# Kernel optimization log

Measured on AMD Instinct MI355X. Metric: run time of the kernel, lower is better.

Reference implementation:

```python
import jax, jax.numpy as jnp
import numpy as np

SEQ_LEN = 1632   # L, divisible by K=12, Locc=4, mmse_block=12
UP = 8           # number of (user, port) entries (flattened dict)
B = 32           # batch_size
A = 64           # num_rx_ant
K = 12           # ktc=4 -> K=12
LOCC = 4         # ktc=4 -> Locc=4
BLK = 12         # mmse_block_size
SEARCH = 10      # delay_search_range = (-10, 10)
RHO = 0.9        # exponential channel-correlation model for default C matrix


def setup_inputs() -> dict:
    key = jax.random.key(0)
    k1, k2, k3 = jax.random.split(key, 3)
    return {
        "ls_real": jax.random.normal(k1, (UP, B, A, SEQ_LEN), jnp.float32),
        "ls_imag": jax.random.normal(k2, (UP, B, A, SEQ_LEN), jnp.float32),
        "cyclic_shifts": jax.random.randint(k3, (UP,), 0, K, dtype=jnp.int32),
    }


def _estimate_entry(ls, n_u_p):
    """Full per-(user,port) pipeline. ls: [B, A, L] complex64, n_u_p: scalar int."""
    L = ls.shape[-1]
    bsz, nant = ls.shape[0], ls.shape[1]
    ideal_peak = ((K - n_u_p) % K) * (L // K)           # scalar int

    # --- IFFT to time domain + per-sample power summed over antennas ---
    h_time = jnp.fft.ifft(ls, axis=-1)                   # [B, A, L]
    pwr = jnp.sum(jnp.abs(h_time) ** 2, axis=1)          # [B, L]

    # --- timing-offset search in a window around the ideal peak ---
    offsets = jnp.arange(-SEARCH, SEARCH + 1)            # [21]
    idxs = (ideal_peak + offsets) % L                    # [21]
    window = pwr[:, idxs]                                # [B, 21]
    toff = offsets[jnp.argmax(window, axis=1)]           # [B] int
    m = toff + ideal_peak                                # [B] int

    # --- phasor correction exp(j 2 pi m n / L) (modular for precision) ---
    nvec = jnp.arange(L)
    ang = (2.0 * jnp.pi / L) * ((m[:, None] * nvec[None, :]) % L).astype(jnp.float32)
    phas_m = jnp.exp(1j * ang)                           # [B, L] complex64
    h_shift = ls * phas_m[:, None, :]                    # [B, A, L]

    # --- OCC demux: average groups of Locc ---
    red = L // LOCC
    h_avg = h_shift.reshape(bsz, nant, red, LOCC).mean(axis=-1)  # [B, A, L/4]

    # --- linear interpolation back to length L (np.interp semantics) ---
    # original sample positions: (LOCC-1)/2 + i*LOCC  (uniform grid)
    t = jnp.arange(L, dtype=jnp.float32)
    p = jnp.clip((t - (LOCC - 1) / 2.0) / LOCC, 0.0, red - 1.0)  # clamped -> edge hold
    i0 = jnp.clip(jnp.floor(p).astype(jnp.int32), 0, red - 2)
    frac = (p - i0.astype(jnp.float32))                  # [L] real
    h_interp = (jnp.take(h_avg, i0, axis=-1) * (1.0 - frac)
                + jnp.take(h_avg, i0 + 1, axis=-1) * frac)       # [B, A, L]

    # torch code computes this under no_grad -> block gradients
    h_wr = jax.lax.stop_gradient(h_interp)

    # --- noise power estimated from frequency-domain LS estimate ---
    d = ls[..., 1:] - ls[..., :-1]
    noise_pw = jnp.mean(jnp.abs(d) ** 2, axis=(1, 2)) / 2.0      # [B]

    # --- block MMSE filter: W = C (C + sigma^2 I)^-1, C = rho^|i-j| ---
    ii = jnp.arange(BLK)
    C = (RHO ** jnp.abs(ii[:, None] - ii[None, :])).astype(jnp.float32)  # [12,12]
    eye = jnp.eye(BLK, dtype=jnp.float32)
    inv = jax.vmap(lambda s: jnp.linalg.inv(C + s * eye))(noise_pw)       # [B,12,12]
    W = jnp.einsum('ij,bjk->bik', C, inv).astype(jnp.complex64)           # [B,12,12]

    hb = h_wr.reshape(bsz, nant, L // BLK, BLK)
    out = jnp.einsum('bij,banj->bani', W, hb).reshape(bsz, nant, L)
    return out


def reference(ls_real, ls_imag, cyclic_shifts):
    ls = ls_real + 1j * ls_imag                          # [UP, B, A, L] complex64
    out = jax.vmap(_estimate_entry)(ls, cyclic_shifts)   # [UP, B, A, L] complex64
    return jnp.stack([out.real, out.imag], axis=-1)      # [UP, B, A, L, 2] float32
```

## Files before the change

kernel.cpp:

```cpp
#include <hip/hip_runtime.h>
#include <math.h>

#define L 1632
#define NUP 8
#define NB 32
#define NA 64
#define KK 12
#define NW 21
#define RED 408

__global__ __launch_bounds__(256) void k1_window(
    const float* __restrict__ lsr, const float* __restrict__ lsi,
    const int* __restrict__ cshift,
    float* __restrict__ winp, float* __restrict__ noisep)
{
    const int bid   = blockIdx.x;
    const int ub    = bid >> 4;
    const int chunk = bid & 15;
    const int u     = ub >> 5;
    const int tid   = threadIdx.x;
    const int wave  = tid >> 6;
    const int lane  = tid & 63;
    const int a     = chunk * 4 + wave;
    const int row   = (ub * NA + a) * L;

    const int shift = cshift[u];
    const int ip    = ((KK - shift) % KK) * (L / KK);
    int t0 = ip - 10;
    t0 = ((t0 % L) + L) % L;

    const float cph = (float)(2.0 * M_PI / (double)L);

    float accr[NW], acci[NW];
#pragma unroll
    for (int o = 0; o < NW; o++) { accr[o] = 0.0f; acci[o] = 0.0f; }
    float na = 0.0f;
    float carry_r = 0.0f, carry_i = 0.0f;

#define ELEM(XR, XI, N) { \
    const int idx0 = ((N) * t0) % L; \
    float s0, c0, s1, c1; \
    __sincosf(cph * (float)idx0, &s0, &c0); \
    __sincosf(cph * (float)(N),  &s1, &c1); \
    float yr = (XR) * c0 - (XI) * s0; \
    float yi = (XR) * s0 + (XI) * c0; \
    _Pragma("unroll") \
    for (int o = 0; o < NW; o++) { \
        accr[o] += yr; acci[o] += yi; \
        const float t_ = yr * c1 - yi * s1; \
        yi = yr * s1 + yi * c1; yr = t_; } }

    for (int k = 0; k < 7; k++) {
        const int nb  = 256 * k + 4 * lane;
        const bool act = (nb < L);
        float4 xr = make_float4(0.f, 0.f, 0.f, 0.f);
        float4 xi = make_float4(0.f, 0.f, 0.f, 0.f);
        if (act) {
            xr = *reinterpret_cast<const float4*>(lsr + row + nb);
            xi = *reinterpret_cast<const float4*>(lsi + row + nb);
        }
        const float c63r = __shfl(carry_r, 63);
        const float c63i = __shfl(carry_i, 63);
        const float upr  = __shfl_up(xr.w, 1);
        const float upi  = __shfl_up(xi.w, 1);
        const float pr   = (lane == 0) ? c63r : upr;
        const float pi   = (lane == 0) ? c63i : upi;
        if (act) {
            if (!(k == 0 && lane == 0)) {
                const float dr = xr.x - pr, di = xi.x - pi; na += dr * dr + di * di;
            }
            { const float dr = xr.y - xr.x, di = xi.y - xi.x; na += dr * dr + di * di; }
            { const float dr = xr.z - xr.y, di = xi.z - xi.y; na += dr * dr + di * di; }
            { const float dr = xr.w - xr.z, di = xi.w - xi.z; na += dr * dr + di * di; }
        }
        carry_r = xr.w; carry_i = xi.w;
        ELEM(xr.x, xi.x, nb + 0)
        ELEM(xr.y, xi.y, nb + 1)
        ELEM(xr.z, xi.z, nb + 2)
        ELEM(xr.w, xi.w, nb + 3)
    }
#undef ELEM

#pragma unroll
    for (int m = 1; m < 64; m <<= 1) {
#pragma unroll
        for (int o = 0; o < NW; o++) {
            accr[o] += __shfl_xor(accr[o], m);
            acci[o] += __shfl_xor(acci[o], m);
        }
        na += __shfl_xor(na, m);
    }

    if (lane == 0) {
#pragma unroll
        for (int o = 0; o < NW; o++)
            atomicAdd(&winp[ub * NW + o], accr[o] * accr[o] + acci[o] * acci[o]);
        atomicAdd(&noisep[ub], na);
    }
}

__global__ __launch_bounds__(192) void k2_wmat(
    const float* __restrict__ winp, const float* __restrict__ noisep,
    const int* __restrict__ cshift,
    float* __restrict__ Wout, int* __restrict__ mmOut)
{
    const int ub  = blockIdx.x;
    const int u   = ub >> 5;
    const int tid = threadIdx.x;
    __shared__ float win[NW];
    __shared__ float Cs[12][12];
    __shared__ float aug[12][25];
    __shared__ float snoise;

    if (tid < NW) win[tid] = winp[ub * NW + tid];
    if (tid == NW) snoise = noisep[ub] / (float)NA / (float)(L - 1) / 2.0f;
    if (tid >= 32 && tid < 32 + 144) {
        const int t = tid - 32;
        const int i = t / 12, j = t % 12;
        const int d = (i > j) ? (i - j) : (j - i);
        double v = 1.0;
        for (int k = 0; k < d; k++) v *= 0.9;
        Cs[i][j] = (float)v;
    }
    __syncthreads();

    if (tid < 144) {
        const int i = tid / 12, j = tid % 12;
        aug[i][j]      = Cs[i][j] + ((i == j) ? snoise : 0.0f);
        aug[i][12 + j] = (i == j) ? 1.0f : 0.0f;
    }
    __syncthreads();

    for (int k = 0; k < 12; k++) {
        float pv = 1.0f, rowkj = 0.0f;
        float fcol[12];
        if (tid < 24) {
            pv    = aug[k][k];
            rowkj = aug[k][tid];
#pragma unroll
            for (int i = 0; i < 12; i++) fcol[i] = aug[i][k];
        }
        __syncthreads();
        if (tid < 24) {
            const float nrm = rowkj / pv;
            aug[k][tid] = nrm;
#pragma unroll
            for (int i = 0; i < 12; i++)
                if (i != k) aug[i][tid] -= fcol[i] * nrm;
        }
        __syncthreads();
    }

    if (tid == 0) {
        float best = win[0];
        int bo = 0;
        for (int o = 1; o < NW; o++)
            if (win[o] > best) { best = win[o]; bo = o; }
        const int shift = cshift[u];
        const int ip = ((KK - shift) % KK) * (L / KK);
        const int m = ip + (bo - 10);
        mmOut[ub] = ((m % L) + L) % L;
    }

    if (tid < 144) {
        const int i = tid / 12, j = tid % 12;
        float w = 0.0f;
#pragma unroll
        for (int k = 0; k < 12; k++) w += Cs[i][k] * aug[k][12 + j];
        Wout[ub * 144 + tid] = w;
    }
}

__global__ __launch_bounds__(256) void k3_main(
    const float* __restrict__ lsr, const float* __restrict__ lsi,
    const float* __restrict__ Wall, const int* __restrict__ mmArr,
    float* __restrict__ out)
{
    const int bid = blockIdx.x;
    const int ub  = bid >> 6;
    const int row = bid * L;
    const int tid = threadIdx.x;
    __shared__ float2 havg[RED];
    __shared__ float2 hint[L];
    __shared__ float  Wl[144];
    if (tid < 144) Wl[tid] = Wall[ub * 144 + tid];
    const int mm = mmArr[ub];
    const float cph = (float)(2.0 * M_PI / (double)L);

    for (int r = tid; r < RED; r += 256) {
        const int base = 4 * r;
        const float4 xr = *reinterpret_cast<const float4*>(lsr + row + base);
        const float4 xi = *reinterpret_cast<const float4*>(lsi + row + base);
        int idx = (mm * base) % L;
        float ar = 0.0f, ai = 0.0f, sn, cs;
        __sincosf(cph * (float)idx, &sn, &cs);
        ar += xr.x * cs - xi.x * sn; ai += xr.x * sn + xi.x * cs;
        idx += mm; if (idx >= L) idx -= L;
        __sincosf(cph * (float)idx, &sn, &cs);
        ar += xr.y * cs - xi.y * sn; ai += xr.y * sn + xi.y * cs;
        idx += mm; if (idx >= L) idx -= L;
        __sincosf(cph * (float)idx, &sn, &cs);
        ar += xr.z * cs - xi.z * sn; ai += xr.z * sn + xi.z * cs;
        idx += mm; if (idx >= L) idx -= L;
        __sincosf(cph * (float)idx, &sn, &cs);
        ar += xr.w * cs - xi.w * sn; ai += xr.w * sn + xi.w * cs;
        havg[r] = make_float2(ar * 0.25f, ai * 0.25f);
    }
    __syncthreads();

    for (int t = tid; t < L; t += 256) {
        float p = ((float)t - 1.5f) * 0.25f;
        p = fminf(fmaxf(p, 0.0f), 407.0f);
        int i0 = (int)p;
        if (i0 > 406) i0 = 406;
        const float fr = p - (float)i0;
        const float2 h0 = havg[i0], h1 = havg[i0 + 1];
        hint[t] = make_float2(h0.x * (1.0f - fr) + h1.x * fr,
                              h0.y * (1.0f - fr) + h1.y * fr);
    }
    __syncthreads();

    float2* o2 = reinterpret_cast<float2*>(out);
    for (int e = tid; e < L; e += 256) {
        const int j = e / 12;
        const int i = e - j * 12;
        const float* wr = &Wl[i * 12];
        float ax = 0.0f, ay = 0.0f;
#pragma unroll
        for (int k = 0; k < 12; k++) {
            const float  w = wr[k];
            const float2 h = hint[j * 12 + k];
            ax += w * h.x; ay += w * h.y;
        }
        o2[row + e] = make_float2(ax, ay);
    }
}

extern "C" void kernel_launch(void* const* d_in, const int* in_sizes, int n_in,
                              void* d_out, int out_size, void* d_ws, size_t ws_size,
                              hipStream_t stream) {
    const float* lsr    = (const float*)d_in[0];
    const float* lsi    = (const float*)d_in[1];
    const int*   cshift = (const int*)d_in[2];
    float* out = (float*)d_out;

    char* ws = (char*)d_ws;
    float* Wout   = (float*)(ws);
    float* winp   = (float*)(ws + 147456);
    float* noisep = (float*)(ws + 147456 + 21504);
    int*   mmArr  = (int*)  (ws + 147456 + 21504 + 1024);

    hipMemsetAsync(winp, 0, 21504 + 1024, stream);

    hipLaunchKernelGGL(k1_window, dim3(NUP * NB * 16), dim3(256), 0, stream,
                       lsr, lsi, cshift, winp, noisep);
    hipLaunchKernelGGL(k2_wmat, dim3(NUP * NB), dim3(192), 0, stream,
                       winp, noisep, cshift, Wout, mmArr);
    hipLaunchKernelGGL(k3_main, dim3(NUP * NB * NA), dim3(256), 0, stream,
                       lsr, lsi, Wout, mmArr, out);
}
```

Baseline: 504.8 us.

## Compute windowed DFT via radix-4 split with shared-memory twiddle table

The k1 window kernel now splits each row into four quarter segments, combines them with a radix-4 butterfly, and evaluates the 21 DFT bins against a precomputed cos/sin table kept in shared memory. This replaces the per-element sincos calls and the 21-step rotation recurrence of the old version. Each block now handles one (user,batch) pair across all 64 antennas, with 8 waves each doing 8 antennas, so the per-bin results are reduced in shared memory and written directly. That removes the global atomics and the memset. The cost is a large shared-memory table (about 68KB) and only 256 blocks of 512 threads, which may leave the GPU underoccupied.

After: 605.6 us. +20.0%, slower.

```diff
diff --git a/kernel.cpp b/kernel.cpp
--- a/kernel.cpp
+++ b/kernel.cpp
@@ -8,21 +8,23 @@
 #define KK 12
 #define NW 21
 #define RED 408
-
-__global__ __launch_bounds__(256) void k1_window(
+#define WS 408
+#define WIM (NW*WS)
+
+__global__ __launch_bounds__(512, 2) void k1_window(
     const float* __restrict__ lsr, const float* __restrict__ lsi,
     const int* __restrict__ cshift,
     float* __restrict__ winp, float* __restrict__ noisep)
 {
-    const int bid   = blockIdx.x;
-    const int ub    = bid >> 4;
-    const int chunk = bid & 15;
-    const int u     = ub >> 5;
-    const int tid   = threadIdx.x;
-    const int wave  = tid >> 6;
-    const int lane  = tid & 63;
-    const int a     = chunk * 4 + wave;
-    const int row   = (ub * NA + a) * L;
+    const int ub   = blockIdx.x;
+    const int u    = ub >> 5;
+    const int tid  = threadIdx.x;
+    const int wave = tid >> 6;
+    const int lane = tid & 63;
+
+    __shared__ float WT[2 * NW * WS];
+    __shared__ float win[NW];
+    __shared__ float nshared;
 
     const int shift = cshift[u];
     const int ip    = ((KK - shift) % KK) * (L / KK);
@@ -31,72 +33,168 @@
 
     const float cph = (float)(2.0 * M_PI / (double)L);
 
-    float accr[NW], acci[NW];
-#pragma unroll
-    for (int o = 0; o < NW; o++) { accr[o] = 0.0f; acci[o] = 0.0f; }
+    for (int f = tid; f < NW * WS; f += 512) {
+        const int o = f / WS;
+        const int s = f - o * WS;
+        const int t = (t0 + o) % L;
+        const int idx = (s * t) % L;
+        float sn, cs;
+        __sincosf(cph * (float)idx, &sn, &cs);
+        WT[f]       = cs;
+        WT[WIM + f] = sn;
+    }
+    if (tid < NW)  win[tid] = 0.0f;
+    if (tid == NW) nshared = 0.0f;
+    __syncthreads();
+
+    const int c4 = t0 & 3;
+
+    float winacc[NW];
+#pragma unroll
+    for (int o = 0; o < NW; o++) winacc[o] = 0.0f;
     float na = 0.0f;
-    float carry_r = 0.0f, carry_i = 0.0f;
-
-#define ELEM(XR, XI, N) { \
-    const int idx0 = ((N) * t0) % L; \
-    float s0, c0, s1, c1; \
-    __sincosf(cph * (float)idx0, &s0, &c0); \
-    __sincosf(cph * (float)(N),  &s1, &c1); \
-    float yr = (XR) * c0 - (XI) * s0; \
-    float yi = (XR) * s0 + (XI) * c0; \
-    _Pragma("unroll") \
-    for (int o = 0; o < NW; o++) { \
-        accr[o] += yr; acci[o] += yi; \
-        const float t_ = yr * c1 - yi * s1; \
-        yi = yr * s1 + yi * c1; yr = t_; } }
-
-    for (int k = 0; k < 7; k++) {
-        const int nb  = 256 * k + 4 * lane;
-        const bool act = (nb < L);
-        float4 xr = make_float4(0.f, 0.f, 0.f, 0.f);
-        float4 xi = make_float4(0.f, 0.f, 0.f, 0.f);
-        if (act) {
-            xr = *reinterpret_cast<const float4*>(lsr + row + nb);
-            xi = *reinterpret_cast<const float4*>(lsi + row + nb);
-        }
-        const float c63r = __shfl(carry_r, 63);
-        const float c63i = __shfl(carry_i, 63);
-        const float upr  = __shfl_up(xr.w, 1);
-        const float upi  = __shfl_up(xi.w, 1);
-        const float pr   = (lane == 0) ? c63r : upr;
-        const float pi   = (lane == 0) ? c63i : upi;
-        if (act) {
-            if (!(k == 0 && lane == 0)) {
-                const float dr = xr.x - pr, di = xi.x - pi; na += dr * dr + di * di;
-            }
-            { const float dr = xr.y - xr.x, di = xi.y - xi.x; na += dr * dr + di * di; }
-            { const float dr = xr.z - xr.y, di = xi.z - xi.y; na += dr * dr + di * di; }
-            { const float dr = xr.w - xr.z, di = xi.w - xi.z; na += dr * dr + di * di; }
-        }
-        carry_r = xr.w; carry_i = xi.w;
-        ELEM(xr.x, xi.x, nb + 0)
-        ELEM(xr.y, xi.y, nb + 1)
-        ELEM(xr.z, xi.z, nb + 2)
-        ELEM(xr.w, xi.w, nb + 3)
-    }
-#undef ELEM
-
-#pragma unroll
-    for (int m = 1; m < 64; m <<= 1) {
-#pragma unroll
-        for (int o = 0; o < NW; o++) {
-            accr[o] += __shfl_xor(accr[o], m);
-            acci[o] += __shfl_xor(acci[o], m);
-        }
-        na += __shfl_xor(na, m);
-    }
+
+    for (int i = 0; i < 8; i++) {
+        const int a   = wave * 8 + i;
+        const int row = (ub * NA + a) * L;
+
+        float accr[NW], acci[NW];
+#pragma unroll
+        for (int o = 0; o < NW; o++) { accr[o] = 0.0f; acci[o] = 0.0f; }
+
+        float s255r[4], s255i[4], s0r[4], s0i[4], s407r[4], s407i[4];
+
+        for (int j = 0; j < 2; j++) {
+            const int  nact = j ? 38 : 64;
+            const bool act  = lane < nact;
+            const int  s0   = 256 * j + 4 * lane;
+            const int  sc   = act ? s0 : 0;
+
+            float exr[4][4], exi[4][4];
+#pragma unroll
+            for (int q = 0; q < 4; q++) {
+#pragma unroll
+                for (int e = 0; e < 4; e++) { exr[q][e] = 0.0f; exi[q][e] = 0.0f; }
+                if (act) {
+                    const float4 r4 = *reinterpret_cast<const float4*>(lsr + row + 408 * q + s0);
+                    const float4 i4 = *reinterpret_cast<const float4*>(lsi + row + 408 * q + s0);
+                    exr[q][0] = r4.x; exr[q][1] = r4.y; exr[q][2] = r4.z; exr[q][3] = r4.w;
+                    exi[q][0] = i4.x; exi[q][1] = i4.y; exi[q][2] = i4.z; exi[q][3] = i4.w;
+                }
+            }
+
+            if (act) {
+#pragma unroll
+                for (int q = 0; q < 4; q++) {
+                    float dr, di;
+                    dr = exr[q][1] - exr[q][0]; di = exi[q][1] - exi[q][0]; na += dr * dr + di * di;
+                    dr = exr[q][2] - exr[q][1]; di = exi[q][2] - exi[q][1]; na += dr * dr + di * di;
+                    dr = exr[q][3] - exr[q][2]; di = exi[q][3] - exi[q][2]; na += dr * dr + di * di;
+                }
+            }
+#pragma unroll
+            for (int q = 0; q < 4; q++) {
+                const float pr = __shfl_up(exr[q][3], 1);
+                const float pi = __shfl_up(exi[q][3], 1);
+                if (j == 0) {
+                    if (lane > 0) {
+                        const float dr = exr[q][0] - pr, di = exi[q][0] - pi;
+                        na += dr * dr + di * di;
+                    }
+                    s255r[q] = __shfl(exr[q][3], 63); s255i[q] = __shfl(exi[q][3], 63);
+                    s0r[q]   = __shfl(exr[q][0], 0);  s0i[q]   = __shfl(exi[q][0], 0);
+                } else {
+                    const float qr = (lane == 0) ? s255r[q] : pr;
+                    const float qi = (lane == 0) ? s255i[q] : pi;
+                    if (act) {
+                        const float dr = exr[q][0] - qr, di = exi[q][0] - qi;
+                        na += dr * dr + di * di;
+                    }
+                    s407r[q] = __shfl(exr[q][3], 37); s407i[q] = __shfl(exi[q][3], 37);
+                }
+            }
+
+            float Gr[4][4], Gi[4][4];
+#pragma unroll
+            for (int e = 0; e < 4; e++) {
+                const float x0r = exr[0][e], x0i = exi[0][e];
+                const float x1r = exr[1][e], x1i = exi[1][e];
+                const float x2r = exr[2][e], x2i = exi[2][e];
+                const float x3r = exr[3][e], x3i = exi[3][e];
+                const float ar = x0r + x2r, ai = x0i + x2i;
+                const float br = x0r - x2r, bi = x0i - x2i;
+                const float cr = x1r + x3r, ci = x1i + x3i;
+                const float dr = x1r - x3r, di = x1i - x3i;
+                Gr[e][0] = ar + cr; Gi[e][0] = ai + ci;
+                Gr[e][2] = ar - cr; Gi[e][2] = ai - ci;
+                Gr[e][1] = br - di; Gi[e][1] = bi + dr;
+                Gr[e][3] = br + di; Gi[e][3] = bi - dr;
+            }
+
+            float Hr[4][4], Hi[4][4];
+#define RELAB(C) { _Pragma("unroll") \
+            for (int e = 0; e < 4; e++) { \
+                Hr[e][0] = Gr[e][(0+(C))&3]; Hi[e][0] = Gi[e][(0+(C))&3]; \
+                Hr[e][1] = Gr[e][(1+(C))&3]; Hi[e][1] = Gi[e][(1+(C))&3]; \
+                Hr[e][2] = Gr[e][(2+(C))&3]; Hi[e][2] = Gi[e][(2+(C))&3]; \
+                Hr[e][3] = Gr[e][(3+(C))&3]; Hi[e][3] = Gi[e][(3+(C))&3]; } }
+            switch (c4) {
+                case 0: RELAB(0); break;
+                case 1: RELAB(1); break;
+                case 2: RELAB(2); break;
+                default: RELAB(3); break;
+            }
+#undef RELAB
+
+#pragma unroll
+            for (int o = 0; o < NW; o++) {
+                const int tau = o & 3;
+                const float4 wr4 = *reinterpret_cast<const float4*>(&WT[o * WS + sc]);
+                const float4 wi4 = *reinterpret_cast<const float4*>(&WT[WIM + o * WS + sc]);
+                accr[o] += wr4.x * Hr[0][tau] - wi4.x * Hi[0][tau]
+                         + wr4.y * Hr[1][tau] - wi4.y * Hi[1][tau]
+                         + wr4.z * Hr[2][tau] - wi4.z * Hi[2][tau]
+                         + wr4.w * Hr[3][tau] - wi4.w * Hi[3][tau];
+                acci[o] += wr4.x * Hi[0][tau] + wi4.x * Hr[0][tau]
+                         + wr4.y * Hi[1][tau] + wi4.y * Hr[1][tau]
+                         + wr4.z * Hi[2][tau] + wi4.z * Hr[2][tau]
+                         + wr4.w * Hi[3][tau] + wi4.w * Hr[3][tau];
+            }
+        }
+
+        if (lane == 0) {
+#pragma unroll
+            for (int q = 1; q < 4; q++) {
+                const float dr = s0r[q] - s407r[q - 1];
+                const float di = s0i[q] - s407i[q - 1];
+                na += dr * dr + di * di;
+            }
+        }
+
+#pragma unroll
+        for (int m = 1; m < 64; m <<= 1) {
+#pragma unroll
+            for (int o = 0; o < NW; o++) {
+                accr[o] += __shfl_xor(accr[o], m);
+                acci[o] += __shfl_xor(acci[o], m);
+            }
+        }
+#pragma unroll
+        for (int o = 0; o < NW; o++)
+            winacc[o] += accr[o] * accr[o] + acci[o] * acci[o];
+    }
+
+#pragma unroll
+    for (int m = 1; m < 64; m <<= 1) na += __shfl_xor(na, m);
 
     if (lane == 0) {
-#pragma unroll
-        for (int o = 0; o < NW; o++)
-            atomicAdd(&winp[ub * NW + o], accr[o] * accr[o] + acci[o] * acci[o]);
-        atomicAdd(&noisep[ub], na);
-    }
+        atomicAdd(&nshared, na);
+#pragma unroll
+        for (int o = 0; o < NW; o++) atomicAdd(&win[o], winacc[o]);
+    }
+    __syncthreads();
+    if (tid < NW)  winp[ub * NW + tid] = win[tid];
+    if (tid == 0)  noisep[ub] = nshared;
 }
 
 __global__ __launch_bounds__(192) void k2_wmat(
@@ -250,9 +348,7 @@
     float* noisep = (float*)(ws + 147456 + 21504);
     int*   mmArr  = (int*)  (ws + 147456 + 21504 + 1024);
 
-    hipMemsetAsync(winp, 0, 21504 + 1024, stream);
-
-    hipLaunchKernelGGL(k1_window, dim3(NUP * NB * 16), dim3(256), 0, stream,
+    hipLaunchKernelGGL(k1_window, dim3(NUP * NB), dim3(512), 0, stream,
                        lsr, lsi, cshift, winp, noisep);
     hipLaunchKernelGGL(k2_wmat, dim3(NUP * NB), dim3(192), 0, stream,
                        winp, noisep, cshift, Wout, mmArr);
```
